# Optimization experiments

Measured on AMD Instinct MI355X. Metric: run time of the kernel, lower is better.

Reference implementation:

```python
import jax, jax.numpy as jnp
import numpy as np

LOW_BAND = 131050.0
HIGH_BAND = 131100.0


def setup_inputs() -> dict:
    key = jax.random.key(0)
    probability = jax.random.normal(key, (64, 2, 512, 512), dtype=jnp.float32)
    return {"probability": probability}


def reference(probability):
    # Original applies softmax when channel-sums don't average to 1; inputs here
    # are raw logits, so the softmax branch is always taken.
    p = jax.nn.softmax(probability, axis=1)
    # per-image foreground pixel mass: [B]
    s = p[:, 1, :, :].sum(axis=(-1, -2))
    B = s.shape[0]

    # Faithful reproduction of the original (buggy) Python loop:
    #  - s_i >= high : appends scalar (s_i - high)^2            -> 1 entry
    #  - s_i <= low  : appends the FULL vector (s - low)^2       -> B entries
    #  - otherwise   : appends scalar 0                          -> 1 entry
    # Final result = total_sum / (total_len - 1); initial zero entry cancels the -1.
    low_vec_sum = ((s - LOW_BAND) ** 2).sum()  # contribution of the whole-batch vector
    contrib = jnp.where(
        s >= HIGH_BAND,
        (s - HIGH_BAND) ** 2,
        jnp.where(s <= LOW_BAND, low_vec_sum, 0.0),
    )
    counts = jnp.where(
        s >= HIGH_BAND,
        1,
        jnp.where(s <= LOW_BAND, B, 1),
    )
    return contrib.sum() / counts.sum().astype(contrib.dtype)
```

## Files before the change

kernel.cpp:

```cpp
#include <hip/hip_runtime.h>
#include <math.h>

constexpr int B       = 64;
constexpr int HW      = 512 * 512;
constexpr int CHUNKS  = 32;
constexpr int PIX     = HW / CHUNKS;
constexpr int THREADS = 256;

__global__ __launch_bounds__(THREADS)
void lb_partials(const float* __restrict__ prob, float* __restrict__ partials) {
    const int blk = blockIdx.x;
    const int b   = blk >> 5;
    const int c   = blk & (CHUNKS - 1);

    const float4* __restrict__ x0 =
        reinterpret_cast<const float4*>(prob + (size_t)b * 2 * HW + (size_t)c * PIX);
    const float4* __restrict__ x1 =
        reinterpret_cast<const float4*>(prob + (size_t)b * 2 * HW + HW + (size_t)c * PIX);

    constexpr int N4 = PIX / 4;
    float acc = 0.f;
    for (int i = threadIdx.x; i < N4; i += THREADS) {
        float4 a = x0[i];
        float4 d = x1[i];
        acc += 1.f / (1.f + expf(a.x - d.x));
        acc += 1.f / (1.f + expf(a.y - d.y));
        acc += 1.f / (1.f + expf(a.z - d.z));
        acc += 1.f / (1.f + expf(a.w - d.w));
    }

    #pragma unroll
    for (int off = 32; off > 0; off >>= 1)
        acc += __shfl_down(acc, off, 64);

    __shared__ float sdata[THREADS / 64];
    const int lane = threadIdx.x & 63;
    const int wid  = threadIdx.x >> 6;
    if (lane == 0) sdata[wid] = acc;
    __syncthreads();
    if (threadIdx.x == 0) {
        float s = 0.f;
        #pragma unroll
        for (int w = 0; w < THREADS / 64; ++w) s += sdata[w];
        partials[blk] = s;
    }
}

__global__ __launch_bounds__(64)
void lb_final(const float* __restrict__ partials, float* __restrict__ out) {
    const int b = threadIdx.x;
    double s = 0.0;
    #pragma unroll
    for (int c = 0; c < CHUNKS; ++c) s += (double)partials[b * CHUNKS + c];

    const double LOW  = 131050.0;
    const double HIGH = 131100.0;

    double dl  = s - LOW;
    double lvs = dl * dl;
    #pragma unroll
    for (int off = 32; off > 0; off >>= 1) lvs += __shfl_xor(lvs, off, 64);

    double contrib, count;
    if (s >= HIGH)      { double d = s - HIGH; contrib = d * d; count = 1.0; }
    else if (s <= LOW)  { contrib = lvs;                        count = (double)B; }
    else                { contrib = 0.0;                        count = 1.0; }

    double cs = contrib, cn = count;
    #pragma unroll
    for (int off = 32; off > 0; off >>= 1) {
        cs += __shfl_xor(cs, off, 64);
        cn += __shfl_xor(cn, off, 64);
    }
    if (b == 0) out[0] = (float)(cs / cn);
}

extern "C" void kernel_launch(void* const* d_in, const int* in_sizes, int n_in,
                              void* d_out, int out_size, void* d_ws, size_t ws_size,
                              hipStream_t stream) {
    const float* prob     = (const float*)d_in[0];
    float*       out      = (float*)d_out;
    float*       partials = (float*)d_ws;

    lb_partials<<<B * CHUNKS, THREADS, 0, stream>>>(prob, partials);
    lb_final<<<1, 64, 0, stream>>>(partials, out);
}
```

Measured before the change: 28.62 us.

## Batch all loads up front, use fast exp/rcp, parallelize final reduction

The partials kernel now issues all eight float4 loads per channel before any math, so more memory requests are in flight per thread. The sigmoid uses __expf and the hardware reciprocal instead of precise expf and division, which cuts ALU work at some cost in accuracy. The final kernel spreads the 32-partial sum per image across four lanes and combines them through a shuffle and shared memory. Holding the loaded data in registers raises register pressure and may lower occupancy.

```diff
diff --git a/kernel.cpp b/kernel.cpp
--- a/kernel.cpp
+++ b/kernel.cpp
@@ -6,6 +6,8 @@
 constexpr int CHUNKS  = 32;
 constexpr int PIX     = HW / CHUNKS;
 constexpr int THREADS = 256;
+constexpr int NBLK    = B * CHUNKS;
+constexpr int ITER    = PIX / 4 / THREADS;
 
 __global__ __launch_bounds__(THREADS)
 void lb_partials(const float* __restrict__ prob, float* __restrict__ partials) {
@@ -18,15 +20,21 @@
     const float4* __restrict__ x1 =
         reinterpret_cast<const float4*>(prob + (size_t)b * 2 * HW + HW + (size_t)c * PIX);
 
-    constexpr int N4 = PIX / 4;
+    float4 a[ITER], d[ITER];
+    #pragma unroll
+    for (int it = 0; it < ITER; ++it) {
+        const int i = it * THREADS + threadIdx.x;
+        a[it] = x0[i];
+        d[it] = x1[i];
+    }
+
     float acc = 0.f;
-    for (int i = threadIdx.x; i < N4; i += THREADS) {
-        float4 a = x0[i];
-        float4 d = x1[i];
-        acc += 1.f / (1.f + expf(a.x - d.x));
-        acc += 1.f / (1.f + expf(a.y - d.y));
-        acc += 1.f / (1.f + expf(a.z - d.z));
-        acc += 1.f / (1.f + expf(a.w - d.w));
+    #pragma unroll
+    for (int it = 0; it < ITER; ++it) {
+        acc += __builtin_amdgcn_rcpf(1.f + __expf(a[it].x - d[it].x));
+        acc += __builtin_amdgcn_rcpf(1.f + __expf(a[it].y - d[it].y));
+        acc += __builtin_amdgcn_rcpf(1.f + __expf(a[it].z - d[it].z));
+        acc += __builtin_amdgcn_rcpf(1.f + __expf(a[it].w - d[it].w));
     }
 
     #pragma unroll
@@ -46,12 +54,24 @@
     }
 }
 
-__global__ __launch_bounds__(64)
+__global__ __launch_bounds__(256)
 void lb_final(const float* __restrict__ partials, float* __restrict__ out) {
-    const int b = threadIdx.x;
-    double s = 0.0;
+    __shared__ double s_sh[B];
+    const int t = threadIdx.x;
+    const int b = t >> 2;
+    const int q = t & 3;
+
+    double ps = 0.0;
     #pragma unroll
-    for (int c = 0; c < CHUNKS; ++c) s += (double)partials[b * CHUNKS + c];
+    for (int k = 0; k < 8; ++k)
+        ps += (double)partials[b * CHUNKS + q * 8 + k];
+    ps += __shfl_xor(ps, 1, 64);
+    ps += __shfl_xor(ps, 2, 64);
+    if (q == 0) s_sh[b] = ps;
+    __syncthreads();
+
+    if (t >= 64) return;
+    const double s = s_sh[t];
 
     const double LOW  = 131050.0;
     const double HIGH = 131100.0;
@@ -62,9 +82,9 @@
     for (int off = 32; off > 0; off >>= 1) lvs += __shfl_xor(lvs, off, 64);
 
     double contrib, count;
-    if (s >= HIGH)      { double d = s - HIGH; contrib = d * d; count = 1.0; }
-    else if (s <= LOW)  { contrib = lvs;                        count = (double)B; }
-    else                { contrib = 0.0;                        count = 1.0; }
+    if (s >= HIGH)      { double dd = s - HIGH; contrib = dd * dd; count = 1.0; }
+    else if (s <= LOW)  { contrib = lvs;                           count = (double)B; }
+    else                { contrib = 0.0;                           count = 1.0; }
 
     double cs = contrib, cn = count;
     #pragma unroll
@@ -72,7 +92,7 @@
         cs += __shfl_xor(cs, off, 64);
         cn += __shfl_xor(cn, off, 64);
     }
-    if (b == 0) out[0] = (float)(cs / cn);
+    if (t == 0) out[0] = (float)(cs / cn);
 }
 
 extern "C" void kernel_launch(void* const* d_in, const int* in_sizes, int n_in,
@@ -82,6 +102,6 @@
     float*       out      = (float*)d_out;
     float*       partials = (float*)d_ws;
 
-    lb_partials<<<B * CHUNKS, THREADS, 0, stream>>>(prob, partials);
-    lb_final<<<1, 64, 0, stream>>>(partials, out);
+    lb_partials<<<NBLK, THREADS, 0, stream>>>(prob, partials);
+    lb_final<<<1, 256, 0, stream>>>(partials, out);
 }
```

Measured after the change: 27.18 us. -5.0%, faster.
